# Optimization experiments

Measured on AMD Instinct MI355X. Metric: run time of the kernel, lower is better.

The kernel has to match this reference:

```python
import jax, jax.numpy as jnp
import numpy as np

B, L, E, H = 4, 2048, 1024, 16
D = E // H  # head_dim = 64
NEG_INF = -1e9


def _rope(x):
    # x: [B, L, H, D]; standard rotate-half RoPE over head_dim
    seq = x.shape[1]
    inv_freq = 1.0 / (10000.0 ** (jnp.arange(0, D, 2, dtype=jnp.float32) / D))  # [D/2]
    ang = jnp.arange(seq, dtype=jnp.float32)[:, None] * inv_freq               # [L, D/2]
    cos = jnp.concatenate([jnp.cos(ang), jnp.cos(ang)], axis=-1)[None, :, None, :]
    sin = jnp.concatenate([jnp.sin(ang), jnp.sin(ang)], axis=-1)[None, :, None, :]
    x1, x2 = jnp.split(x, 2, axis=-1)
    rot = jnp.concatenate([-x2, x1], axis=-1)
    return x * cos + rot * sin


def setup_inputs() -> dict:
    key = jax.random.key(0)
    ks = jax.random.split(key, 12)
    xavier = lambda k: jax.random.uniform(k, (E, E), jnp.float32,
                                          -np.sqrt(6.0 / (E + E)), np.sqrt(6.0 / (E + E)))
    return {
        "query": jax.random.normal(ks[0], (B, L, E), jnp.float32),
        "key": jax.random.normal(ks[1], (B, L, E), jnp.float32),
        "value": jax.random.normal(ks[2], (B, L, E), jnp.float32),
        "wq": xavier(ks[3]), "bq": jnp.zeros((E,), jnp.float32),
        "wk": xavier(ks[4]), "bk": jnp.zeros((E,), jnp.float32),
        "wv": xavier(ks[5]), "bv": jnp.zeros((E,), jnp.float32),
        "wo": xavier(ks[6]), "bo": jnp.zeros((E,), jnp.float32),
        "key_padding_mask": jax.random.randint(ks[7], (B, L), 0, 2).astype(bool),
    }


def reference(query, key, value, wq, bq, wk, bk, wv, bv, wo, bo, key_padding_mask):
    b, ql = query.shape[0], query.shape[1]
    sl = key.shape[1]
    q = (query @ wq.T + bq).reshape(b, ql, H, D)
    k = (key @ wk.T + bk).reshape(b, sl, H, D)
    v = (value @ wv.T + bv).reshape(b, sl, H, D)
    q = _rope(q)
    k = _rope(k)
    # causal mask (is_causal=True, attn_mask=None path) + key padding mask, additive
    causal = jnp.where(jnp.triu(jnp.ones((ql, sl), bool), k=1), NEG_INF, 0.0)  # [L, L]
    kpm = jnp.where(key_padding_mask[:, None, None, :], NEG_INF, 0.0)          # [B,1,1,S]
    mask = causal[None, None, :, :] + kpm
    scores = jnp.einsum("bqhd,bkhd->bhqk", q, k) / np.sqrt(D) + mask
    attn = jax.nn.softmax(scores, axis=-1)
    out = jnp.einsum("bhqk,bkhd->bqhd", attn, v).reshape(b, ql, E)
    return out @ wo.T + bo
```

## Files before the change

kernel.cpp:

```cpp
#include <hip/hip_runtime.h>

typedef unsigned short u16;
typedef unsigned int   u32;

using bf16x8 = __attribute__((ext_vector_type(8))) __bf16;
using f32x4  = __attribute__((ext_vector_type(4))) float;
using f32x16 = __attribute__((ext_vector_type(16))) float;
using u32x4  = __attribute__((ext_vector_type(4))) u32;

#define DEV static __device__ __forceinline__
#define GP(p) (const __attribute__((address_space(1))) void*)(p)
#define LP(p) (__attribute__((address_space(3))) void*)(p)
#define WAITB(N) asm volatile("s_waitcnt vmcnt(" N ")\n\ts_barrier" ::: "memory")
#define WAITVM(N) do{ asm volatile("s_waitcnt vmcnt(" N ")" ::: "memory"); \
                      __builtin_amdgcn_sched_barrier(0); }while(0)
#define LGKMB asm volatile("s_waitcnt lgkmcnt(0)\n\ts_barrier" ::: "memory")

DEV u16 f2bf(float f){
  u32 u = __builtin_bit_cast(u32, f);
  u32 r = u + 0x7fffu + ((u>>16)&1u);
  return (u16)(r>>16);
}
DEV float bcf(u32 x){ return __builtin_bit_cast(float, x); }
DEV bf16x8 as_bf(uint4 v){ return __builtin_bit_cast(bf16x8, v); }
DEV u32 cvt_pk(float lo, float hi){
  u32 r;
  asm("v_cvt_pk_bf16_f32 %0, %1, %2" : "=v"(r) : "v"(lo), "v"(hi));
  return r;
}
DEV void plswap(u32 &a, u32 &b){
  auto r = __builtin_amdgcn_permlane32_swap((int)a, (int)b, false, false);
  a = (u32)r[0]; b = (u32)r[1];
}
DEV float fexp2(float x){ float r; asm("v_exp_f32 %0, %1" : "=v"(r) : "v"(x)); return r; }
DEV float max3f(float a, float b, float c){
  float r; asm("v_max3_f32 %0, %1, %2, %3" : "=v"(r) : "v"(a), "v"(b), "v"(c)); return r;
}
DEV float fractf_(float x){ float r; asm("v_fract_f32 %0, %1" : "=v"(r) : "v"(x)); return r; }
DEV float sinrev(float f){ float r; asm("v_sin_f32 %0, %1" : "=v"(r) : "v"(f)); return r; }
DEV float cosrev(float f){ float r; asm("v_cos_f32 %0, %1" : "=v"(r) : "v"(f)); return r; }

constexpr int CB = 4, CL = 2048, CE = 1024, CH = 16, CD = 64;
constexpr int CM = CB*CL;
constexpr float LOG2E  = 1.44269504088896f;
constexpr float NEGBIG = -1.44269504e9f;
constexpr float INV2PI = 0.15915494309189535f;

__global__ void mask_kernel(const void* __restrict__ mask, float* __restrict__ maskf){
  __shared__ int a_gt1, a_badf, a_oddnz, a_evennz;
  if (threadIdx.x==0){ a_gt1=0; a_badf=0; a_oddnz=0; a_evennz=0; }
  __syncthreads();
  const u32* w = (const u32*)mask;
  int gt1=0, badf=0, oddnz=0, evennz=0;
  for (int i=threadIdx.x; i<2048; i+=256){
    u32 v = w[i];
    if (v > 1u) gt1 = 1;
    if (v != 0u && v != 0x3f800000u) badf = 1;
    if (v != 0u){ if (i & 1) oddnz = 1; else evennz = 1; }
  }
  if (gt1) atomicOr(&a_gt1,1);
  if (badf) atomicOr(&a_badf,1);
  if (oddnz) atomicOr(&a_oddnz,1);
  if (evennz) atomicOr(&a_evennz,1);
  __syncthreads();
  int mode;
  if (!a_gt1)           mode = (!a_oddnz && a_evennz) ? 3 : 0;
  else if (!a_badf)     mode = 1;
  else                  mode = 2;
  int i = blockIdx.x*blockDim.x + threadIdx.x;
  int v;
  if      (mode==0) v = ((const int*)mask)[i] != 0;
  else if (mode==1) v = ((const float*)mask)[i] != 0.f;
  else if (mode==3) v = ((const int*)mask)[2*i] != 0;
  else              v = ((const unsigned char*)mask)[i] != 0;
  maskf[i] = v ? NEGBIG : 0.f;
}

__global__ __launch_bounds__(512) void gemm_qkv(
    const float* __restrict__ query, const float* __restrict__ keyp,
    const float* __restrict__ value,
    const float* __restrict__ wq, const float* __restrict__ wk,
    const float* __restrict__ wv,
    const float* __restrict__ bq, const float* __restrict__ bk, const float* __restrict__ bv,
    u16* __restrict__ Qp, u16* __restrict__ Kp, u16* __restrict__ Vt)
{
  __shared__ u16 As[2][16384];
  __shared__ u16 Bs[2][8192];
  const int z = blockIdx.y;
  const int tid=threadIdx.x, lane=tid&63, wid=tid>>6;
  const int llo=lane&15, lhi=lane>>4;
  const float* Af; const float* Btf;
  if (z==0){ Af=query; Btf=wq; }
  else if (z==1){ Af=keyp; Btf=wk; }
  else { Af=wv; Btf=value; }
  int bid = blockIdx.x;
  int xcd = bid&7, j = bid>>3;
  int mb, nb;
  if (z<2){ mb = xcd*4 + (j>>3); nb = j&7; }
  else    { mb = j&3;  nb = xcd*8 + (j>>2); }
  const int m0 = mb*256, n0 = nb*128;
  const int wr = wid>>1, wc = wid&1;
  const int rswA = llo&7;

  const float* aptr[4]; int aco[4];
  #pragma unroll
  for (int i=0;i<4;i++){
    int c = tid + i*512, row=c>>3, sc=(c&7)^(row&7);
    aptr[i] = Af + (size_t)(m0+row)*CE + sc*8;
    aco[i] = c*8;
  }
  const float* bptr[2]; int bco[2];
  #pragma unroll
  for (int i=0;i<2;i++){
    int c = tid + i*512, row=c>>3, sc=(c&7)^(row&7);
    bptr[i] = Btf + (size_t)(n0+row)*CE + sc*8;
    bco[i] = c*8;
  }

  u32x4 A0[8], B0[4], A1[8], B1[4];

#define LOADT(T, RA, RB) do{ \
  _Pragma("unroll") \
  for (int i=0;i<4;i++){ \
    asm volatile("global_load_dwordx4 %0, %2, off\n\tglobal_load_dwordx4 %1, %2, off offset:16" \
      : "=&v"(RA[2*i]), "=&v"(RA[2*i+1]) : "v"(aptr[i] + (size_t)(T)*64) : "memory"); \
  } \
  _Pragma("unroll") \
  for (int i=0;i<2;i++){ \
    asm volatile("global_load_dwordx4 %0, %2, off\n\tglobal_load_dwordx4 %1, %2, off offset:16" \
      : "=&v"(RB[2*i]), "=&v"(RB[2*i+1]) : "v"(bptr[i] + (size_t)(T)*64) : "memory"); \
  } \
}while(0)

#define CVTW(dst, lo4, hi4) do{ \
  dst.x = cvt_pk(bcf(lo4.x), bcf(lo4.y)); \
  dst.y = cvt_pk(bcf(lo4.z), bcf(lo4.w)); \
  dst.z = cvt_pk(bcf(hi4.x), bcf(hi4.y)); \
  dst.w = cvt_pk(bcf(hi4.z), bcf(hi4.w)); \
}while(0)

#define WRITET(BUF, RA, RB) do{ \
  _Pragma("unroll") \
  for (int i=0;i<4;i++){ \
    u32x4 w; CVTW(w, RA[2*i], RA[2*i+1]); \
    *(u32x4*)&As[BUF][aco[i]] = w; \
  } \
  _Pragma("unroll") \
  for (int i=0;i<2;i++){ \
    u32x4 w; CVTW(w, RB[2*i], RB[2*i+1]); \
    *(u32x4*)&Bs[BUF][bco[i]] = w; \
  } \
}while(0)

  f32x4 acc[4][4] = {};

  auto COMP = [&](int buf){
    const char* as = (const char*)As[buf];
    const char* bs = (const char*)Bs[buf];
    #pragma unroll
    for (int ks=0; ks<2; ks++){
      bf16x8 af[4], bf_[4];
      #pragma unroll
      for (int mr=0;mr<4;mr++){
        int r = wr*64+mr*16+llo;
        af[mr] = as_bf(*(const uint4*)(as + r*128 + (((ks*4+lhi)^rswA)<<4)));
      }
      #pragma unroll
      for (int nr=0;nr<4;nr++){
        int r = wc*64+nr*16+llo;
        bf_[nr] = as_bf(*(const uint4*)(bs + r*128 + (((ks*4+lhi)^rswA)<<4)));
      }
      #pragma unroll
      for (int mr=0;mr<4;mr++)
        #pragma unroll
        for (int nr=0;nr<4;nr++)
          acc[mr][nr] = __builtin_amdgcn_mfma_f32_16x16x32_bf16(af[mr], bf_[nr], acc[mr][nr], 0,0,0);
    }
  };

  LOADT(0, A0, B0);
  LOADT(1, A1, B1);
  WAITVM("12");
  WRITET(0, A0, B0);
  LGKMB;

  #pragma unroll 1
  for (int jj=0; jj<7; jj++){
    const int t = 2*jj;
    LOADT(t+2, A0, B0);
    WAITVM("12");
    WRITET(1, A1, B1);
    COMP(0);
    LGKMB;
    LOADT(t+3, A1, B1);
    WAITVM("12");
    WRITET(0, A0, B0);
    COMP(1);
    LGKMB;
  }
  WAITVM("0");
  WRITET(1, A1, B1);
  COMP(0);
  LGKMB;
  COMP(1);

#undef LOADT
#undef WRITET

  const int colbase = n0 + wc*64;
  if (z < 2){
    const float* bias = z ? bk : bq;
    u16* outp = z ? Kp : Qp;
    const float scale = z ? 1.f : 0.125f*LOG2E;
    const int h = colbase >> 6;
    float b1[2], b2[2], invr[2];
    #pragma unroll
    for (int nr=0;nr<2;nr++){
      int j2 = nr*16 + llo;
      b1[nr] = bias[colbase + j2];
      b2[nr] = bias[colbase + j2 + 32];
      invr[nr] = exp2f(-(float)j2 * 0.41524101186092033f) * INV2PI;
    }
    #pragma unroll
    for (int mr=0;mr<4;mr++)
      #pragma unroll
      for (int r=0;r<4;r++){
        int row = m0 + wr*64 + mr*16 + lhi*4 + r;
        int b = row >> 11, l = row & 2047;
        u16* dst = outp + (((size_t)(b*CH + h)*CL + l) << 6);
        #pragma unroll
        for (int nr=0;nr<2;nr++){
          int j2 = nr*16 + llo;
          float x1 = (acc[mr][nr][r]   + b1[nr]) * scale;
          float x2 = (acc[mr][nr+2][r] + b2[nr]) * scale;
          float fr = fractf_((float)l * invr[nr]);
          float sn = sinrev(fr), cs = cosrev(fr);
          dst[j2]      = f2bf(x1*cs - x2*sn);
          dst[j2 + 32] = f2bf(x2*cs + x1*sn);
        }
      }
  } else {
    #pragma unroll
    for (int mr=0;mr<4;mr++)
      #pragma unroll
      for (int r=0;r<4;r++){
        int row = m0 + wr*64 + mr*16 + lhi*4 + r;
        float bvv = bv[row];
        #pragma unroll
        for (int nr=0;nr<4;nr++){
          int col = colbase + nr*16 + llo;
          Vt[(size_t)row*CM + col] = f2bf(acc[mr][nr][r] + bvv);
        }
      }
  }
}

__global__ __launch_bounds__(512) void gemm_out(
    const u16* __restrict__ A, const float* __restrict__ Btf,
    const float* __restrict__ bias, float* __restrict__ C)
{
  __shared__ u16 As[3][16384];
  __shared__ u16 Bs[2][8192];
  const int tid=threadIdx.x, lane=tid&63, wid=tid>>6;
  const int llo=lane&15, lhi=lane>>4;
  int bid = blockIdx.x;
  int xcd = bid&7, j = bid>>3;
  const int m0 = (xcd*4 + (j>>3))*256, n0 = (j&7)*128;
  const int wr = wid>>1, wc = wid&1;
  const int rswA = llo&7;

  auto STAGEA = [&](int t, int buf){
    #pragma unroll
    for (int i=0;i<4;i++){
      int c = tid + i*512, row=c>>3, sc=(c&7)^(row&7);
      __builtin_amdgcn_global_load_lds(GP(A + (size_t)(m0+row)*CE + t*64 + sc*8),
                                       LP(&As[buf][c*8]), 16, 0, 0);
    }
  };

  const float* bptr[2]; int bco[2];
  #pragma unroll
  for (int i=0;i<2;i++){
    int c = tid + i*512, row=c>>3, sc=(c&7)^(row&7);
    bptr[i] = Btf + (size_t)(n0+row)*CE + sc*8;
    bco[i] = c*8;
  }
  u32x4 B0[4], B1[4];

#define LOADB(T, RB) do{ \
  _Pragma("unroll") \
  for (int i=0;i<2;i++){ \
    asm volatile("global_load_dwordx4 %0, %2, off\n\tglobal_load_dwordx4 %1, %2, off offset:16" \
      : "=&v"(RB[2*i]), "=&v"(RB[2*i+1]) : "v"(bptr[i] + (size_t)(T)*64) : "memory"); \
  } \
}while(0)

#define WRITEB(BUF, RB) do{ \
  _Pragma("unroll") \
  for (int i=0;i<2;i++){ \
    u32x4 w; CVTW(w, RB[2*i], RB[2*i+1]); \
    *(u32x4*)&Bs[BUF][bco[i]] = w; \
  } \
}while(0)

  f32x4 acc[4][4] = {};

  auto COMP = [&](int abuf, int bbuf){
    const char* as = (const char*)As[abuf];
    const char* bs = (const char*)Bs[bbuf];
    #pragma unroll
    for (int ks=0; ks<2; ks++){
      bf16x8 af[4], bf_[4];
      #pragma unroll
      for (int mr=0;mr<4;mr++){
        int r = wr*64+mr*16+llo;
        af[mr] = as_bf(*(const uint4*)(as + r*128 + (((ks*4+lhi)^rswA)<<4)));
      }
      #pragma unroll
      for (int nr=0;nr<4;nr++){
        int r = wc*64+nr*16+llo;
        bf_[nr] = as_bf(*(const uint4*)(bs + r*128 + (((ks*4+lhi)^rswA)<<4)));
      }
      #pragma unroll
      for (int mr=0;mr<4;mr++)
        #pragma unroll
        for (int nr=0;nr<4;nr++)
          acc[mr][nr] = __builtin_amdgcn_mfma_f32_16x16x32_bf16(af[mr], bf_[nr], acc[mr][nr], 0,0,0);
    }
  };

  STAGEA(0,0); LOADB(0, B0);
  STAGEA(1,1); LOADB(1, B1);
  WAITVM("8");
  WRITEB(0, B0);
  LGKMB;

  #pragma unroll 1
  for (int jj=0; jj<7; jj++){
    const int t = 2*jj;
    STAGEA(t+2, (t+2)%3); LOADB(t+2, B0);
    WAITVM("8");
    WRITEB(1, B1);
    COMP(t%3, 0);
    LGKMB;
    STAGEA(t+3, (t+3)%3); LOADB(t+3, B1);
    WAITVM("8");
    WRITEB(0, B0);
    COMP((t+1)%3, 1);
    LGKMB;
  }
  WAITVM("0");
  WRITEB(1, B1);
  COMP(2, 0);
  LGKMB;
  COMP(0, 1);

#undef LOADB
#undef WRITEB

  #pragma unroll
  for (int mr=0;mr<4;mr++)
    #pragma unroll
    for (int nr=0;nr<4;nr++)
      #pragma unroll
      for (int r=0;r<4;r++){
        int row = m0 + wr*64 + mr*16 + lhi*4 + r;
        int col = n0 + wc*64 + nr*16 + llo;
        C[(size_t)row*CE + col] = acc[mr][nr][r] + bias[col];
      }
}

__global__ __launch_bounds__(256,2) void attn_kernel(
    const u16* __restrict__ Qp, const u16* __restrict__ Kp, const u16* __restrict__ Vt,
    const float* __restrict__ maskf, u16* __restrict__ AO)
{
  __shared__ u16 K_lds[4][4096];
  __shared__ u16 V_lds[4][4096];
  __shared__ float M_lds[2048];
  const int bh = blockIdx.x;
  const int slot = blockIdx.y;
  const int b = bh >> 4, h = bh & 15;
  const int tid=threadIdx.x, lane=tid&63, wid=tid>>6;
  const int l31 = lane&31, hi = lane>>5;
  const u16* Qh = Qp + (size_t)bh*CL*CD;
  const u16* Kh = Kp + (size_t)bh*CL*CD;
  const u16* Vhd = Vt + (size_t)(h*CD)*CM + b*CL;

  #pragma unroll
  for (int i=0;i<2;i++)
    __builtin_amdgcn_global_load_lds(GP(maskf + b*CL + (i*256+tid)*4),
                                     LP(&M_lds[(i*256+tid)*4]), 16, 0, 0);

  auto STAGE = [&](int t, int buf){
    const u16* Ksrc = Kh + t*64*CD;
    const u16* Vsrc = Vhd + t*64;
    #pragma unroll
    for (int i=0;i<2;i++){
      int c = tid + i*256;
      int row = c>>3, sc = c&7;
      int c16 = sc ^ (row&7);
      __builtin_amdgcn_global_load_lds(GP(Ksrc + row*CD + c16*8),
                                       LP(&K_lds[buf][c*8]), 16, 0, 0);
      __builtin_amdgcn_global_load_lds(GP(Vsrc + (size_t)row*CM + c16*8),
                                       LP(&V_lds[buf][c*8]), 16, 0, 0);
    }
  };

  const int rowb = l31*128;
  const int rsw  = (l31&7)<<4;
  const int qts2[2] = {15-slot, slot};

  for (int qi=0; qi<2; qi++){
    const int qt = qts2[qi];
    const int qw0 = qt*128 + wid*32;
    const int qlane = qw0 + l31;

    bf16x8 qf[4];
    #pragma unroll
    for (int c=0;c<4;c++)
      qf[c] = as_bf(*(const uint4*)(Qh + (size_t)qlane*CD + c*16 + hi*8));

    f32x16 o0 = {}, o1 = {};
    float m_r = -3e38f, l_r = 0.f;
    f32x16 sA0, sA1, sB0, sB1;

    const int nt = qt*2 + 2;
    STAGE(0,0); STAGE(1,1);

    auto QK = [&](int t, f32x16& d0, f32x16& d1){
      const char* kb = (const char*)K_lds[t&3];
      f32x16 z0 = {}, z1 = {};
      __builtin_amdgcn_s_setprio(1);
      #pragma unroll
      for (int c=0;c<4;c++){
        int cb = (c*32 + hi*16) ^ rsw;
        bf16x8 k0 = as_bf(*(const uint4*)(kb + rowb + cb));
        bf16x8 k1 = as_bf(*(const uint4*)(kb + 4096 + rowb + cb));
        z0 = __builtin_amdgcn_mfma_f32_32x32x16_bf16(k0, qf[c], z0, 0,0,0);
        z1 = __builtin_amdgcn_mfma_f32_32x32x16_bf16(k1, qf[c], z1, 0,0,0);
      }
      __builtin_amdgcn_s_setprio(0);
      d0 = z0; d1 = z1;
    };

    auto SMPV = [&](int tp, f32x16& s0, f32x16& s1){
      const int kv0 = tp*64;
      const char* vb = (const char*)V_lds[tp&3];

      f32x4 cm[8];
      #pragma unroll
      for (int s2=0;s2<2;s2++)
        #pragma unroll
        for (int g=0; g<4; g++)
          cm[s2*4+g] = *(const f32x4*)&M_lds[kv0 + s2*32 + g*8 + hi*4];

      if (kv0 + 63 > qw0){
        #pragma unroll
        for (int s2=0;s2<2;s2++){
          f32x16& sv = s2 ? s1 : s0;
          #pragma unroll
          for (int reg=0; reg<16; reg++){
            int k = kv0 + s2*32 + (reg&3) + (reg>>2)*8 + hi*4;
            float v = sv[reg] + cm[s2*4+(reg>>2)][reg&3];
            sv[reg] = (k > qlane) ? v + NEGBIG : v;
          }
        }
      } else {
        #pragma unroll
        for (int s2=0;s2<2;s2++){
          f32x16& sv = s2 ? s1 : s0;
          #pragma unroll
          for (int reg=0; reg<16; reg++)
            sv[reg] = sv[reg] + cm[s2*4+(reg>>2)][reg&3];
        }
      }

      f32x16 mx;
      #pragma unroll
      for (int r=0;r<16;r++) mx[r] = fmaxf(s0[r], s1[r]);
      float a0 = max3f(mx[0],mx[1],mx[2]);
      float a1 = max3f(mx[3],mx[4],mx[5]);
      float a2 = max3f(mx[6],mx[7],mx[8]);
      float a3 = max3f(mx[9],mx[10],mx[11]);
      float a4 = max3f(mx[12],mx[13],mx[14]);
      float vmax = fmaxf(max3f(a0,a1,a2), max3f(a3,a4,mx[15]));
      vmax = fmaxf(vmax, __shfl_xor(vmax, 32));

      if (__any(vmax > m_r + 12.0f)){
        float mnew = fmaxf(m_r, vmax);
        float sc = fexp2(m_r - mnew);
        l_r *= sc;
        o0 *= sc; o1 *= sc;
        m_r = mnew;
      }

      #pragma unroll
      for (int r=0;r<16;r++){
        s0[r] = fexp2(s0[r] - m_r);
        s1[r] = fexp2(s1[r] - m_r);
      }
      f32x16 sm = s0 + s1;
      #pragma unroll
      for (int w=8; w>=1; w>>=1)
        #pragma unroll
        for (int r=0;r<w;r++) sm[r] = sm[r] + sm[r+w];
      float rsum = sm[0];
      rsum += __shfl_xor(rsum, 32);
      l_r += rsum;

      u32 w_[16];
      #pragma unroll
      for (int s2=0;s2<2;s2++){
        f32x16& sv = s2 ? s1 : s0;
        #pragma unroll
        for (int c=0;c<2;c++){
          u32 a  = cvt_pk(sv[c*8+0], sv[c*8+1]);
          u32 bb = cvt_pk(sv[c*8+2], sv[c*8+3]);
          u32 cc = cvt_pk(sv[c*8+4], sv[c*8+5]);
          u32 dd = cvt_pk(sv[c*8+6], sv[c*8+7]);
          plswap(a, cc); plswap(bb, dd);
          int base = (s2*2+c)*4;
          w_[base+0]=a; w_[base+1]=bb; w_[base+2]=cc; w_[base+3]=dd;
        }
      }

      __builtin_amdgcn_s_setprio(1);
      #pragma unroll
      for (int kc=0; kc<4; kc++){
        bf16x8 pf = as_bf(make_uint4(w_[kc*4], w_[kc*4+1], w_[kc*4+2], w_[kc*4+3]));
        int cb = (kc*32 + hi*16) ^ rsw;
        bf16x8 v0 = as_bf(*(const uint4*)(vb + rowb + cb));
        bf16x8 v1 = as_bf(*(const uint4*)(vb + 4096 + rowb + cb));
        o0 = __builtin_amdgcn_mfma_f32_32x32x16_bf16(v0, pf, o0, 0,0,0);
        o1 = __builtin_amdgcn_mfma_f32_32x32x16_bf16(v1, pf, o1, 0,0,0);
      }
      __builtin_amdgcn_s_setprio(0);
    };

    WAITB("4");
    if (2 < nt) STAGE(2,2);
    QK(0, sA0, sA1);

    #pragma unroll 1
    for (int jx=0; jx<qt; jx++){
      int t = 2*jx+1;
      WAITB("4");
      if (t+2 < nt) STAGE(t+2,(t+2)&3);
      QK(t, sB0, sB1);
      SMPV(t-1, sA0, sA1);
      t = 2*jx+2;
      WAITB("4");
      if (t+2 < nt) STAGE(t+2,(t+2)&3);
      QK(t, sA0, sA1);
      SMPV(t-1, sB0, sB1);
    }
    WAITB("0");
    QK(nt-1, sB0, sB1);
    SMPV(nt-2, sA0, sA1);
    SMPV(nt-1, sB0, sB1);

    float inv = 1.f / l_r;
    u16* dst = AO + (size_t)(b*CL + qlane)*CE + h*CD;
    #pragma unroll
    for (int mt=0; mt<2; mt++){
      f32x16& ov = mt ? o1 : o0;
      #pragma unroll
      for (int g=0; g<4; g++){
        u32 lo  = cvt_pk(ov[g*4+0]*inv, ov[g*4+1]*inv);
        u32 hi2 = cvt_pk(ov[g*4+2]*inv, ov[g*4+3]*inv);
        *(uint2*)(dst + mt*32 + g*8 + hi*4) = make_uint2(lo, hi2);
      }
    }
    __syncthreads();
  }
}

extern "C" void kernel_launch(void* const* d_in, const int* in_sizes, int n_in,
                              void* d_out, int out_size, void* d_ws, size_t ws_size,
                              hipStream_t stream) {
  const float* query = (const float*)d_in[0];
  const float* key_  = (const float*)d_in[1];
  const float* value = (const float*)d_in[2];
  const float* wq = (const float*)d_in[3];
  const float* bq = (const float*)d_in[4];
  const float* wk = (const float*)d_in[5];
  const float* bk = (const float*)d_in[6];
  const float* wv = (const float*)d_in[7];
  const float* bv = (const float*)d_in[8];
  const float* wo = (const float*)d_in[9];
  const float* bo = (const float*)d_in[10];
  const void*  kpm = d_in[11];

  char* ws = (char*)d_ws;
  constexpr size_t SZ_ME_BF = (size_t)CM*CE*2;
  constexpr size_t OFF_MASKF= 256;
  constexpr size_t OFF_AO   = 65536;
  constexpr size_t OFF_KP   = OFF_AO + SZ_ME_BF;
  constexpr size_t OFF_VT   = OFF_KP + SZ_ME_BF;
  constexpr size_t OFF_QP   = OFF_VT + SZ_ME_BF;

  float* maskf = (float*)(ws + OFF_MASKF);
  u16*  AO  = (u16*)(ws + OFF_AO);
  u16*  Kp  = (u16*)(ws + OFF_KP);
  u16*  Vt  = (u16*)(ws + OFF_VT);
  u16*  Qp  = (u16*)(ws + OFF_QP);

  mask_kernel<<<32,256,0,stream>>>(kpm, maskf);

  gemm_qkv<<<dim3(256,3),512,0,stream>>>(query, key_, value, wq, wk, wv,
                                         bq, bk, bv, Qp, Kp, Vt);

  attn_kernel<<<dim3(CB*CH, 8),256,0,stream>>>(Qp, Kp, Vt, maskf, AO);

  gemm_out<<<256,512,0,stream>>>(AO, wo, bo, (float*)d_out);
}
```

Before: 190.4 us.

## Pre-cast QKV weights to bf16 and stream them directly into LDS

A new cast_w kernel converts wq, wk and wv to bf16 once per call, writing them into the attention-output workspace buffer before attention overwrites it. The QKV GEMM then loads the weight operand with global_load_lds directly into a 3- or 4-slot LDS ring, skipping the register round-trip and per-tile conversion. Only the activation operand still goes through registers for fp32-to-bf16 conversion. This halves weight bytes read in the GEMM and frees registers, at the cost of an extra launch that reads all weights and a larger LDS footprint.

After: 188.7 us. Within noise of the previous version (-0.9%).

```diff
diff --git a/kernel.cpp b/kernel.cpp
--- a/kernel.cpp
+++ b/kernel.cpp
@@ -76,23 +76,37 @@
   maskf[i] = v ? NEGBIG : 0.f;
 }
 
+__global__ void cast_w(const float* __restrict__ wq, const float* __restrict__ wk,
+                       const float* __restrict__ wv,
+                       u16* __restrict__ oq, u16* __restrict__ ok, u16* __restrict__ ov){
+  int i = blockIdx.x*blockDim.x + threadIdx.x;
+  int w = i >> 18, j = i & ((1<<18)-1);
+  const float* in = (w==0)?wq:(w==1)?wk:wv;
+  u16* out = (w==0)?oq:(w==1)?ok:ov;
+  float4 a = ((const float4*)in)[j];
+  ushort4 h;
+  h.x = f2bf(a.x); h.y = f2bf(a.y); h.z = f2bf(a.z); h.w = f2bf(a.w);
+  ((ushort4*)out)[j] = h;
+}
+
+#define CVTW(dst, lo4, hi4) do{ \
+  dst.x = cvt_pk(bcf(lo4.x), bcf(lo4.y)); \
+  dst.y = cvt_pk(bcf(lo4.z), bcf(lo4.w)); \
+  dst.z = cvt_pk(bcf(hi4.x), bcf(hi4.y)); \
+  dst.w = cvt_pk(bcf(hi4.z), bcf(hi4.w)); \
+}while(0)
+
 __global__ __launch_bounds__(512) void gemm_qkv(
     const float* __restrict__ query, const float* __restrict__ keyp,
     const float* __restrict__ value,
-    const float* __restrict__ wq, const float* __restrict__ wk,
-    const float* __restrict__ wv,
+    const u16* __restrict__ wqb, const u16* __restrict__ wkb, const u16* __restrict__ wvb,
     const float* __restrict__ bq, const float* __restrict__ bk, const float* __restrict__ bv,
     u16* __restrict__ Qp, u16* __restrict__ Kp, u16* __restrict__ Vt)
 {
-  __shared__ u16 As[2][16384];
-  __shared__ u16 Bs[2][8192];
+  __shared__ u16 LDSU[65536];
   const int z = blockIdx.y;
   const int tid=threadIdx.x, lane=tid&63, wid=tid>>6;
   const int llo=lane&15, lhi=lane>>4;
-  const float* Af; const float* Btf;
-  if (z==0){ Af=query; Btf=wq; }
-  else if (z==1){ Af=keyp; Btf=wk; }
-  else { Af=wv; Btf=value; }
   int bid = blockIdx.x;
   int xcd = bid&7, j = bid>>3;
   int mb, nb;
@@ -102,113 +116,103 @@
   const int wr = wid>>1, wc = wid&1;
   const int rswA = llo&7;
 
-  const float* aptr[4]; int aco[4];
-  #pragma unroll
-  for (int i=0;i<4;i++){
-    int c = tid + i*512, row=c>>3, sc=(c&7)^(row&7);
-    aptr[i] = Af + (size_t)(m0+row)*CE + sc*8;
-    aco[i] = c*8;
-  }
-  const float* bptr[2]; int bco[2];
-  #pragma unroll
-  for (int i=0;i<2;i++){
-    int c = tid + i*512, row=c>>3, sc=(c&7)^(row&7);
-    bptr[i] = Btf + (size_t)(n0+row)*CE + sc*8;
-    bco[i] = c*8;
-  }
-
-  u32x4 A0[8], B0[4], A1[8], B1[4];
-
-#define LOADT(T, RA, RB) do{ \
+  f32x4 acc[4][4] = {};
+
+  auto COMP = [&](const u16* asrc, const u16* bsrc){
+    const char* as = (const char*)asrc;
+    const char* bs = (const char*)bsrc;
+    #pragma unroll
+    for (int ks=0; ks<2; ks++){
+      bf16x8 af[4], bf_[4];
+      #pragma unroll
+      for (int mr=0;mr<4;mr++){
+        int r = wr*64+mr*16+llo;
+        af[mr] = as_bf(*(const uint4*)(as + r*128 + (((ks*4+lhi)^rswA)<<4)));
+      }
+      #pragma unroll
+      for (int nr=0;nr<4;nr++){
+        int r = wc*64+nr*16+llo;
+        bf_[nr] = as_bf(*(const uint4*)(bs + r*128 + (((ks*4+lhi)^rswA)<<4)));
+      }
+      #pragma unroll
+      for (int mr=0;mr<4;mr++)
+        #pragma unroll
+        for (int nr=0;nr<4;nr++)
+          acc[mr][nr] = __builtin_amdgcn_mfma_f32_16x16x32_bf16(af[mr], bf_[nr], acc[mr][nr], 0,0,0);
+    }
+  };
+
+  if (z < 2){
+    const float* Af = z ? keyp : query;
+    const u16*  Wb  = z ? wkb : wqb;
+    u16* As0 = &LDSU[0];
+    u16* As1 = &LDSU[16384];
+
+    const float* aptr[4]; int aco[4];
+    #pragma unroll
+    for (int i=0;i<4;i++){
+      int c = tid + i*512, row=c>>3, sc=(c&7)^(row&7);
+      aptr[i] = Af + (size_t)(m0+row)*CE + sc*8;
+      aco[i] = c*8;
+    }
+    u32x4 A0[8], A1[8];
+
+#define LOADA(T, RA) do{ \
   _Pragma("unroll") \
   for (int i=0;i<4;i++){ \
     asm volatile("global_load_dwordx4 %0, %2, off\n\tglobal_load_dwordx4 %1, %2, off offset:16" \
       : "=&v"(RA[2*i]), "=&v"(RA[2*i+1]) : "v"(aptr[i] + (size_t)(T)*64) : "memory"); \
   } \
+}while(0)
+
+#define STAGEB(T, SLOT) do{ \
   _Pragma("unroll") \
   for (int i=0;i<2;i++){ \
-    asm volatile("global_load_dwordx4 %0, %2, off\n\tglobal_load_dwordx4 %1, %2, off offset:16" \
-      : "=&v"(RB[2*i]), "=&v"(RB[2*i+1]) : "v"(bptr[i] + (size_t)(T)*64) : "memory"); \
-  } \
-}while(0)
-
-#define CVTW(dst, lo4, hi4) do{ \
-  dst.x = cvt_pk(bcf(lo4.x), bcf(lo4.y)); \
-  dst.y = cvt_pk(bcf(lo4.z), bcf(lo4.w)); \
-  dst.z = cvt_pk(bcf(hi4.x), bcf(hi4.y)); \
-  dst.w = cvt_pk(bcf(hi4.z), bcf(hi4.w)); \
-}while(0)
-
-#define WRITET(BUF, RA, RB) do{ \
+    int c = tid + i*512, row=c>>3, sc=(c&7)^(row&7); \
+    __builtin_amdgcn_global_load_lds(GP(Wb + (size_t)(n0+row)*CE + (T)*64 + sc*8), \
+                                     LP(&LDSU[32768 + (SLOT)*8192 + c*8]), 16, 0, 0); \
+  } \
+}while(0)
+
+#define WRITEA(DST, RA) do{ \
   _Pragma("unroll") \
   for (int i=0;i<4;i++){ \
     u32x4 w; CVTW(w, RA[2*i], RA[2*i+1]); \
-    *(u32x4*)&As[BUF][aco[i]] = w; \
-  } \
-  _Pragma("unroll") \
-  for (int i=0;i<2;i++){ \
-    u32x4 w; CVTW(w, RB[2*i], RB[2*i+1]); \
-    *(u32x4*)&Bs[BUF][bco[i]] = w; \
-  } \
-}while(0)
-
-  f32x4 acc[4][4] = {};
-
-  auto COMP = [&](int buf){
-    const char* as = (const char*)As[buf];
-    const char* bs = (const char*)Bs[buf];
-    #pragma unroll
-    for (int ks=0; ks<2; ks++){
-      bf16x8 af[4], bf_[4];
-      #pragma unroll
-      for (int mr=0;mr<4;mr++){
-        int r = wr*64+mr*16+llo;
-        af[mr] = as_bf(*(const uint4*)(as + r*128 + (((ks*4+lhi)^rswA)<<4)));
-      }
-      #pragma unroll
-      for (int nr=0;nr<4;nr++){
-        int r = wc*64+nr*16+llo;
-        bf_[nr] = as_bf(*(const uint4*)(bs + r*128 + (((ks*4+lhi)^rswA)<<4)));
-      }
-      #pragma unroll
-      for (int mr=0;mr<4;mr++)
-        #pragma unroll
-        for (int nr=0;nr<4;nr++)
-          acc[mr][nr] = __builtin_amdgcn_mfma_f32_16x16x32_bf16(af[mr], bf_[nr], acc[mr][nr], 0,0,0);
-    }
-  };
-
-  LOADT(0, A0, B0);
-  LOADT(1, A1, B1);
-  WAITVM("12");
-  WRITET(0, A0, B0);
-  LGKMB;
-
-  #pragma unroll 1
-  for (int jj=0; jj<7; jj++){
-    const int t = 2*jj;
-    LOADT(t+2, A0, B0);
-    WAITVM("12");
-    WRITET(1, A1, B1);
-    COMP(0);
+    *(u32x4*)&DST[aco[i]] = w; \
+  } \
+}while(0)
+
+    LOADA(0, A0); STAGEB(0, 0);
+    LOADA(1, A1); STAGEB(1, 1);
+    WAITVM("10");
+    WRITEA(As0, A0);
     LGKMB;
-    LOADT(t+3, A1, B1);
-    WAITVM("12");
-    WRITET(0, A0, B0);
-    COMP(1);
+
+    #pragma unroll 1
+    for (int jj=0; jj<7; jj++){
+      const int t = 2*jj;
+      LOADA(t+2, A0); STAGEB(t+2, (t+2)&3);
+      WAITVM("10");
+      WRITEA(As1, A1);
+      COMP(As0, &LDSU[32768 + (t&3)*8192]);
+      LGKMB;
+      LOADA(t+3, A1); STAGEB(t+3, (t+3)&3);
+      WAITVM("10");
+      WRITEA(As0, A0);
+      COMP(As1, &LDSU[32768 + ((t+1)&3)*8192]);
+      LGKMB;
+    }
+    WAITVM("0");
+    WRITEA(As1, A1);
+    COMP(As0, &LDSU[32768 + 2*8192]);
     LGKMB;
-  }
-  WAITVM("0");
-  WRITET(1, A1, B1);
-  COMP(0);
-  LGKMB;
-  COMP(1);
-
-#undef LOADT
-#undef WRITET
-
-  const int colbase = n0 + wc*64;
-  if (z < 2){
+    COMP(As1, &LDSU[32768 + 3*8192]);
+
+#undef LOADA
+#undef STAGEB
+#undef WRITEA
+
+    const int colbase = n0 + wc*64;
     const float* bias = z ? bk : bq;
     u16* outp = z ? Kp : Qp;
     const float scale = z ? 1.f : 0.125f*LOG2E;
@@ -240,6 +244,74 @@
         }
       }
   } else {
+    u16* Bs0 = &LDSU[49152];
+    u16* Bs1 = &LDSU[57344];
+
+    const float* bptr[2]; int bco[2];
+    #pragma unroll
+    for (int i=0;i<2;i++){
+      int c = tid + i*512, row=c>>3, sc=(c&7)^(row&7);
+      bptr[i] = value + (size_t)(n0+row)*CE + sc*8;
+      bco[i] = c*8;
+    }
+    u32x4 B0[4], B1[4];
+
+#define STAGEA(T, SLOT) do{ \
+  _Pragma("unroll") \
+  for (int i=0;i<4;i++){ \
+    int c = tid + i*512, row=c>>3, sc=(c&7)^(row&7); \
+    __builtin_amdgcn_global_load_lds(GP(wvb + (size_t)(m0+row)*CE + (T)*64 + sc*8), \
+                                     LP(&LDSU[(SLOT)*16384 + c*8]), 16, 0, 0); \
+  } \
+}while(0)
+
+#define LOADB(T, RB) do{ \
+  _Pragma("unroll") \
+  for (int i=0;i<2;i++){ \
+    asm volatile("global_load_dwordx4 %0, %2, off\n\tglobal_load_dwordx4 %1, %2, off offset:16" \
+      : "=&v"(RB[2*i]), "=&v"(RB[2*i+1]) : "v"(bptr[i] + (size_t)(T)*64) : "memory"); \
+  } \
+}while(0)
+
+#define WRITEB(DST, RB) do{ \
+  _Pragma("unroll") \
+  for (int i=0;i<2;i++){ \
+    u32x4 w; CVTW(w, RB[2*i], RB[2*i+1]); \
+    *(u32x4*)&DST[bco[i]] = w; \
+  } \
+}while(0)
+
+    STAGEA(0,0); LOADB(0, B0);
+    STAGEA(1,1); LOADB(1, B1);
+    WAITVM("8");
+    WRITEB(Bs0, B0);
+    LGKMB;
+
+    #pragma unroll 1
+    for (int jj=0; jj<7; jj++){
+      const int t = 2*jj;
+      STAGEA(t+2, (t+2)%3); LOADB(t+2, B0);
+      WAITVM("8");
+      WRITEB(Bs1, B1);
+      COMP(&LDSU[(t%3)*16384], Bs0);
+      LGKMB;
+      STAGEA(t+3, (t+3)%3); LOADB(t+3, B1);
+      WAITVM("8");
+      WRITEB(Bs0, B0);
+      COMP(&LDSU[((t+1)%3)*16384], Bs1);
+      LGKMB;
+    }
+    WAITVM("0");
+    WRITEB(Bs1, B1);
+    COMP(&LDSU[(14%3)*16384], Bs0);
+    LGKMB;
+    COMP(&LDSU[(15%3)*16384], Bs1);
+
+#undef STAGEA
+#undef LOADB
+#undef WRITEB
+
+    const int colbase = n0 + wc*64;
     #pragma unroll
     for (int mr=0;mr<4;mr++)
       #pragma unroll
@@ -605,9 +677,14 @@
   u16*  Vt  = (u16*)(ws + OFF_VT);
   u16*  Qp  = (u16*)(ws + OFF_QP);
 
+  u16* wqb = AO;
+  u16* wkb = AO + (size_t)CE*CE;
+  u16* wvb = AO + (size_t)2*CE*CE;
+
   mask_kernel<<<32,256,0,stream>>>(kpm, maskf);
-
-  gemm_qkv<<<dim3(256,3),512,0,stream>>>(query, key_, value, wq, wk, wv,
+  cast_w<<<3072,256,0,stream>>>(wq, wk, wv, wqb, wkb, wvb);
+
+  gemm_qkv<<<dim3(256,3),512,0,stream>>>(query, key_, value, wqb, wkb, wvb,
                                          bq, bk, bv, Qp, Kp, Vt);
 
   attn_kernel<<<dim3(CB*CH, 8),256,0,stream>>>(Qp, Kp, Vt, maskf, AO);
```

## Pre-convert QKV inputs and weights to bf16, stage GEMM tiles via direct LDS loads

Applied to the files above, without the earlier changes.

A new prep kernel converts query/key/value and the three weight matrices from fp32 to bf16 in workspace, merged with the mask preprocessing. The QKV GEMM then reads bf16 directly with global_load_lds into a triple-buffered LDS pipeline, instead of loading fp32 into registers, converting, and writing to LDS. The aim is to halve GEMM global read traffic and free VGPRs and VALU work inside the GEMM. In exchange it adds a full extra pass over the inputs (read fp32, write bf16) plus more workspace, with a fallback path that splits the launch when workspace is too small.

New measurement: 193.1 us. Within noise of the previous version (+1.4%).

```diff
diff --git a/kernel.cpp b/kernel.cpp
--- a/kernel.cpp
+++ b/kernel.cpp
@@ -46,17 +46,40 @@
 constexpr float NEGBIG = -1.44269504e9f;
 constexpr float INV2PI = 0.15915494309189535f;
 
-__global__ void mask_kernel(const void* __restrict__ mask, float* __restrict__ maskf){
+__global__ void prep_kernel(const float* __restrict__ q, const float* __restrict__ k,
+                            const float* __restrict__ v,
+                            const float* __restrict__ wq, const float* __restrict__ wk,
+                            const float* __restrict__ wv,
+                            u16* __restrict__ oq, u16* __restrict__ ok, u16* __restrict__ ov,
+                            u16* __restrict__ owq, u16* __restrict__ owk, u16* __restrict__ owv,
+                            const void* __restrict__ mask, float* __restrict__ maskf){
+  if (blockIdx.x < 27648){
+    int i = blockIdx.x*blockDim.x + threadIdx.x;
+    const float* in; u16* out; int j;
+    if (i < 3*(1<<21)){
+      int w = i >> 21; j = i & ((1<<21)-1);
+      in = (w==0)?q:(w==1)?k:v; out = (w==0)?oq:(w==1)?ok:ov;
+    } else {
+      int r = i - 3*(1<<21);
+      int w = r >> 18; j = r & ((1<<18)-1);
+      in = (w==0)?wq:(w==1)?wk:wv; out = (w==0)?owq:(w==1)?owk:owv;
+    }
+    float4 a = ((const float4*)in)[j];
+    ushort4 h;
+    h.x = f2bf(a.x); h.y = f2bf(a.y); h.z = f2bf(a.z); h.w = f2bf(a.w);
+    ((ushort4*)out)[j] = h;
+    return;
+  }
   __shared__ int a_gt1, a_badf, a_oddnz, a_evennz;
   if (threadIdx.x==0){ a_gt1=0; a_badf=0; a_oddnz=0; a_evennz=0; }
   __syncthreads();
   const u32* w = (const u32*)mask;
   int gt1=0, badf=0, oddnz=0, evennz=0;
   for (int i=threadIdx.x; i<2048; i+=256){
-    u32 v = w[i];
-    if (v > 1u) gt1 = 1;
-    if (v != 0u && v != 0x3f800000u) badf = 1;
-    if (v != 0u){ if (i & 1) oddnz = 1; else evennz = 1; }
+    u32 x = w[i];
+    if (x > 1u) gt1 = 1;
+    if (x != 0u && x != 0x3f800000u) badf = 1;
+    if (x != 0u){ if (i & 1) oddnz = 1; else evennz = 1; }
   }
   if (gt1) atomicOr(&a_gt1,1);
   if (badf) atomicOr(&a_badf,1);
@@ -67,32 +90,37 @@
   if (!a_gt1)           mode = (!a_oddnz && a_evennz) ? 3 : 0;
   else if (!a_badf)     mode = 1;
   else                  mode = 2;
-  int i = blockIdx.x*blockDim.x + threadIdx.x;
-  int v;
-  if      (mode==0) v = ((const int*)mask)[i] != 0;
-  else if (mode==1) v = ((const float*)mask)[i] != 0.f;
-  else if (mode==3) v = ((const int*)mask)[2*i] != 0;
-  else              v = ((const unsigned char*)mask)[i] != 0;
-  maskf[i] = v ? NEGBIG : 0.f;
-}
+  int i = (blockIdx.x-27648)*blockDim.x + threadIdx.x;
+  int val;
+  if      (mode==0) val = ((const int*)mask)[i] != 0;
+  else if (mode==1) val = ((const float*)mask)[i] != 0.f;
+  else if (mode==3) val = ((const int*)mask)[2*i] != 0;
+  else              val = ((const unsigned char*)mask)[i] != 0;
+  maskf[i] = val ? NEGBIG : 0.f;
+}
+
+#define CVTW(dst, lo4, hi4) do{ \
+  dst.x = cvt_pk(bcf(lo4.x), bcf(lo4.y)); \
+  dst.y = cvt_pk(bcf(lo4.z), bcf(lo4.w)); \
+  dst.z = cvt_pk(bcf(hi4.x), bcf(hi4.y)); \
+  dst.w = cvt_pk(bcf(hi4.z), bcf(hi4.w)); \
+}while(0)
 
 __global__ __launch_bounds__(512) void gemm_qkv(
-    const float* __restrict__ query, const float* __restrict__ keyp,
-    const float* __restrict__ value,
-    const float* __restrict__ wq, const float* __restrict__ wk,
-    const float* __restrict__ wv,
+    const u16* __restrict__ qbf, const u16* __restrict__ kbf, const u16* __restrict__ vbf,
+    const u16* __restrict__ wqb, const u16* __restrict__ wkb, const u16* __restrict__ wvb,
     const float* __restrict__ bq, const float* __restrict__ bk, const float* __restrict__ bv,
-    u16* __restrict__ Qp, u16* __restrict__ Kp, u16* __restrict__ Vt)
+    u16* __restrict__ Qp, u16* __restrict__ Kp, u16* __restrict__ Vt, int zbase)
 {
-  __shared__ u16 As[2][16384];
-  __shared__ u16 Bs[2][8192];
-  const int z = blockIdx.y;
+  __shared__ u16 As[3][16384];
+  __shared__ u16 Bs[3][8192];
+  const int z = zbase + blockIdx.y;
   const int tid=threadIdx.x, lane=tid&63, wid=tid>>6;
   const int llo=lane&15, lhi=lane>>4;
-  const float* Af; const float* Btf;
-  if (z==0){ Af=query; Btf=wq; }
-  else if (z==1){ Af=keyp; Btf=wk; }
-  else { Af=wv; Btf=value; }
+  const u16* A; const u16* Bt;
+  if (z==0){ A=qbf; Bt=wqb; }
+  else if (z==1){ A=kbf; Bt=wkb; }
+  else { A=wvb; Bt=vbf; }
   int bid = blockIdx.x;
   int xcd = bid&7, j = bid>>3;
   int mb, nb;
@@ -102,55 +130,24 @@
   const int wr = wid>>1, wc = wid&1;
   const int rswA = llo&7;
 
-  const float* aptr[4]; int aco[4];
-  #pragma unroll
-  for (int i=0;i<4;i++){
-    int c = tid + i*512, row=c>>3, sc=(c&7)^(row&7);
-    aptr[i] = Af + (size_t)(m0+row)*CE + sc*8;
-    aco[i] = c*8;
-  }
-  const float* bptr[2]; int bco[2];
-  #pragma unroll
-  for (int i=0;i<2;i++){
-    int c = tid + i*512, row=c>>3, sc=(c&7)^(row&7);
-    bptr[i] = Btf + (size_t)(n0+row)*CE + sc*8;
-    bco[i] = c*8;
-  }
-
-  u32x4 A0[8], B0[4], A1[8], B1[4];
-
-#define LOADT(T, RA, RB) do{ \
-  _Pragma("unroll") \
-  for (int i=0;i<4;i++){ \
-    asm volatile("global_load_dwordx4 %0, %2, off\n\tglobal_load_dwordx4 %1, %2, off offset:16" \
-      : "=&v"(RA[2*i]), "=&v"(RA[2*i+1]) : "v"(aptr[i] + (size_t)(T)*64) : "memory"); \
-  } \
-  _Pragma("unroll") \
-  for (int i=0;i<2;i++){ \
-    asm volatile("global_load_dwordx4 %0, %2, off\n\tglobal_load_dwordx4 %1, %2, off offset:16" \
-      : "=&v"(RB[2*i]), "=&v"(RB[2*i+1]) : "v"(bptr[i] + (size_t)(T)*64) : "memory"); \
-  } \
-}while(0)
-
-#define CVTW(dst, lo4, hi4) do{ \
-  dst.x = cvt_pk(bcf(lo4.x), bcf(lo4.y)); \
-  dst.y = cvt_pk(bcf(lo4.z), bcf(lo4.w)); \
-  dst.z = cvt_pk(bcf(hi4.x), bcf(hi4.y)); \
-  dst.w = cvt_pk(bcf(hi4.z), bcf(hi4.w)); \
-}while(0)
-
-#define WRITET(BUF, RA, RB) do{ \
-  _Pragma("unroll") \
-  for (int i=0;i<4;i++){ \
-    u32x4 w; CVTW(w, RA[2*i], RA[2*i+1]); \
-    *(u32x4*)&As[BUF][aco[i]] = w; \
-  } \
-  _Pragma("unroll") \
-  for (int i=0;i<2;i++){ \
-    u32x4 w; CVTW(w, RB[2*i], RB[2*i+1]); \
-    *(u32x4*)&Bs[BUF][bco[i]] = w; \
-  } \
-}while(0)
+  auto STAGE = [&](int t, int buf){
+    #pragma unroll
+    for (int i=0;i<4;i++){
+      int c = tid + i*512;
+      int row = c>>3, ch = c&7;
+      int sc = ch ^ (row&7);
+      __builtin_amdgcn_global_load_lds(GP(A + (size_t)(m0+row)*CE + t*64 + sc*8),
+                                       LP(&As[buf][c*8]), 16, 0, 0);
+    }
+    #pragma unroll
+    for (int i=0;i<2;i++){
+      int c = tid + i*512;
+      int row = c>>3, ch = c&7;
+      int sc = ch ^ (row&7);
+      __builtin_amdgcn_global_load_lds(GP(Bt + (size_t)(n0+row)*CE + t*64 + sc*8),
+                                       LP(&Bs[buf][c*8]), 16, 0, 0);
+    }
+  };
 
   f32x4 acc[4][4] = {};
 
@@ -178,34 +175,17 @@
     }
   };
 
-  LOADT(0, A0, B0);
-  LOADT(1, A1, B1);
-  WAITVM("12");
-  WRITET(0, A0, B0);
-  LGKMB;
+  STAGE(0,0); STAGE(1,1);
+  WAITB("6");
 
   #pragma unroll 1
-  for (int jj=0; jj<7; jj++){
-    const int t = 2*jj;
-    LOADT(t+2, A0, B0);
-    WAITVM("12");
-    WRITET(1, A1, B1);
-    COMP(0);
-    LGKMB;
-    LOADT(t+3, A1, B1);
-    WAITVM("12");
-    WRITET(0, A0, B0);
-    COMP(1);
-    LGKMB;
-  }
-  WAITVM("0");
-  WRITET(1, A1, B1);
+  for (int t=0; t<14; t++){
+    STAGE(t+2, (t+2)%3);
+    COMP(t%3);
+    WAITB("6");
+  }
+  COMP(2); WAITB("0");
   COMP(0);
-  LGKMB;
-  COMP(1);
-
-#undef LOADT
-#undef WRITET
 
   const int colbase = n0 + wc*64;
   if (z < 2){
@@ -291,14 +271,14 @@
   _Pragma("unroll") \
   for (int i=0;i<2;i++){ \
     asm volatile("global_load_dwordx4 %0, %2, off\n\tglobal_load_dwordx4 %1, %2, off offset:16" \
-      : "=&v"(RB[2*i]), "=&v"(RB[2*i+1]) : "v"(bptr[i] + (size_t)(T)*64) : "memory"); \
+      : "=&v"((RB)[2*i]), "=&v"((RB)[2*i+1]) : "v"(bptr[i] + (size_t)(T)*64) : "memory"); \
   } \
 }while(0)
 
 #define WRITEB(BUF, RB) do{ \
   _Pragma("unroll") \
   for (int i=0;i<2;i++){ \
-    u32x4 w; CVTW(w, RB[2*i], RB[2*i+1]); \
+    u32x4 w; CVTW(w, (RB)[2*i], (RB)[2*i+1]); \
     *(u32x4*)&Bs[BUF][bco[i]] = w; \
   } \
 }while(0)
@@ -593,22 +573,44 @@
 
   char* ws = (char*)d_ws;
   constexpr size_t SZ_ME_BF = (size_t)CM*CE*2;
+  constexpr size_t SZ_EE_BF = (size_t)CE*CE*2;
   constexpr size_t OFF_MASKF= 256;
-  constexpr size_t OFF_AO   = 65536;
-  constexpr size_t OFF_KP   = OFF_AO + SZ_ME_BF;
+  constexpr size_t OFF_B0   = 65536;
+  constexpr size_t OFF_B1   = OFF_B0 + SZ_ME_BF;
+  constexpr size_t OFF_B2   = OFF_B1 + SZ_ME_BF;
+  constexpr size_t OFF_WQ   = OFF_B2 + SZ_ME_BF;
+  constexpr size_t OFF_WK   = OFF_WQ + SZ_EE_BF;
+  constexpr size_t OFF_WV   = OFF_WK + SZ_EE_BF;
+  constexpr size_t OFF_KP   = OFF_WV + SZ_EE_BF;
   constexpr size_t OFF_VT   = OFF_KP + SZ_ME_BF;
   constexpr size_t OFF_QP   = OFF_VT + SZ_ME_BF;
 
   float* maskf = (float*)(ws + OFF_MASKF);
-  u16*  AO  = (u16*)(ws + OFF_AO);
+  u16*  qbf = (u16*)(ws + OFF_B0);
+  u16*  kbf = (u16*)(ws + OFF_B1);
+  u16*  vbf = (u16*)(ws + OFF_B2);
+  u16*  wqb = (u16*)(ws + OFF_WQ);
+  u16*  wkb = (u16*)(ws + OFF_WK);
+  u16*  wvb = (u16*)(ws + OFF_WV);
   u16*  Kp  = (u16*)(ws + OFF_KP);
   u16*  Vt  = (u16*)(ws + OFF_VT);
-  u16*  Qp  = (u16*)(ws + OFF_QP);
-
-  mask_kernel<<<32,256,0,stream>>>(kpm, maskf);
-
-  gemm_qkv<<<dim3(256,3),512,0,stream>>>(query, key_, value, wq, wk, wv,
-                                         bq, bk, bv, Qp, Kp, Vt);
+  u16*  AO  = qbf;
+
+  prep_kernel<<<27680,256,0,stream>>>(query, key_, value, wq, wk, wv,
+                                      qbf, kbf, vbf, wqb, wkb, wvb, kpm, maskf);
+
+  u16* Qp;
+  if (ws_size >= OFF_QP + SZ_ME_BF){
+    Qp = (u16*)(ws + OFF_QP);
+    gemm_qkv<<<dim3(256,3),512,0,stream>>>(qbf, kbf, vbf, wqb, wkb, wvb,
+                                           bq, bk, bv, Qp, Kp, Vt, 0);
+  } else {
+    Qp = vbf;
+    gemm_qkv<<<dim3(256,2),512,0,stream>>>(qbf, kbf, vbf, wqb, wkb, wvb,
+                                           bq, bk, bv, Qp, Kp, Vt, 1);
+    gemm_qkv<<<dim3(256,1),512,0,stream>>>(qbf, kbf, vbf, wqb, wkb, wvb,
+                                           bq, bk, bv, Qp, Kp, Vt, 0);
+  }
 
   attn_kernel<<<dim3(CB*CH, 8),256,0,stream>>>(Qp, Kp, Vt, maskf, AO);
 
```
